# Optimization experiments

Measured on AMD Instinct MI355X. Metric: run time of the kernel, lower is better.

The kernel has to match this reference:

```python
import jax, jax.numpy as jnp
import numpy as np

B, L, DK, DV, H, DKL, DVL, R = 64, 4096, 128, 128, 4, 64, 128, 128


def setup_inputs() -> dict:
    key = jax.random.key(0)
    ks = jax.random.split(key, 7)
    K = jax.random.normal(ks[0], (B, L, DK), dtype=jnp.float32)
    V = jax.random.normal(ks[1], (B, L, DV), dtype=jnp.float32)
    mask = jax.random.uniform(ks[2], (B, L)) < 0.25
    mask = mask.at[:, 0].set(False)
    # Learned parameters (Wq is zeros at init in the original; use small random
    # values so the softmax is non-degenerate for correctness testing)
    Wq = jax.random.normal(ks[3], (H, DKL), dtype=jnp.float32) * 0.02
    Wk = jax.random.normal(ks[4], (DK, H, DKL), dtype=jnp.float32) / np.sqrt(DK)
    Wv = jax.random.normal(ks[5], (DV, H, DVL), dtype=jnp.float32) / np.sqrt(DV)
    Wo = jax.random.normal(ks[6], (H, DVL, R), dtype=jnp.float32) / np.sqrt(H * DVL)
    return {"K": K, "V": V, "mask": mask, "Wq": Wq, "Wk": Wk, "Wv": Wv, "Wo": Wo}


def reference(K, V, mask, Wq, Wk, Wv, Wo):
    # scale = 1/sqrt(dim_q), dim_q == dim_k
    scale = 1.0 / jnp.sqrt(jnp.asarray(K.shape[-1], K.dtype))
    Kp = jnp.einsum('bld,dhk->blhk', K, Wk)          # (B, L, H, DKL)
    Vp = jnp.einsum('ble,ehv->blhv', V, Wv)          # (B, L, H, DVL)
    QK = jnp.einsum('hk,blhk->blh', Wq, Kp)          # (B, L, H)
    QK = jnp.where(mask[..., None], -jnp.inf, QK)    # mask over set axis L
    w = jax.nn.softmax(scale * QK, axis=-2)          # softmax over L (dim=-2)
    # nanmean over the set axis (masked positions contribute w=0; NaN entries,
    # if present in V, are skipped exactly as torch.nanmean does)
    QKV = jnp.nanmean(w[..., None] * Vp, axis=-3)    # (B, H, DVL)
    return jnp.einsum('bhv,hvr->br', QKV, Wo)        # (B, R)
```

## Files before the change

### kernel.cpp

```cpp
#include <hip/hip_runtime.h>
#include <math.h>

#define BB   64
#define LL   4096
#define DKC  128
#define DVC  128
#define HC   4
#define DKLC 64
#define DVLC 128
#define RC   128

#define NCA  64
#define CA   64

typedef float f4v __attribute__((ext_vector_type(4)));
__device__ __forceinline__ float4 ntload4(const float4* p) {
    f4v v = __builtin_nontemporal_load((const f4v*)p);
    return make_float4(v.x, v.y, v.z, v.w);
}
__device__ __forceinline__ float dot4(float4 a, float4 b) {
    return a.x * b.x + a.y * b.y + a.z * b.z + a.w * b.w;
}

__global__ __launch_bounds__(512) void k_foldq(const float* __restrict__ Wq,
                                               const float* __restrict__ Wk,
                                               float* __restrict__ q) {
    int t = threadIdx.x;
    int h = t >> 7;
    int d = t & 127;
    float acc = 0.f;
#pragma unroll 8
    for (int k = 0; k < DKLC; ++k)
        acc += Wq[h * DKLC + k] * Wk[(d * HC + h) * DKLC + k];
    q[h * DKC + d] = acc;
}

__global__ __launch_bounds__(256) void k_fused(const float* __restrict__ K,
                                               const float* __restrict__ V,
                                               const int*   __restrict__ mask,
                                               const float* __restrict__ q,
                                               float* __restrict__ stats,
                                               float* __restrict__ partWV) {
    const int bid = blockIdx.x;
    const int b   = bid >> 6;
    const int a   = bid & (NCA - 1);
    const int l0  = a * CA;
    const int t   = threadIdx.x;
    const int w   = t >> 6;
    const int ln  = t & 63;
    const int lin = ln & 15;
    const int rh  = ln >> 5;
    const int rowbase = l0 + w * 16;

    const float4* Kb = (const float4*)(K + (long)b * LL * DKC);
    const float4* Vb = (const float4*)(V + (long)b * LL * DVC);

    float4 k0[4], k1[4];
#pragma unroll
    for (int p = 0; p < 4; ++p) {
        int rp = rowbase + p * 4 + (ln >> 4);
        k0[p] = ntload4(&Kb[rp * 32 + lin]);
        k1[p] = ntload4(&Kb[rp * 32 + 16 + lin]);
    }
    float4 vv[8];
#pragma unroll
    for (int it = 0; it < 8; ++it) {
        int rv = rowbase + it * 2 + rh;
        vv[it] = ntload4(&Vb[rv * 32 + (ln & 31)]);
    }
    int mk[4];
#pragma unroll
    for (int p = 0; p < 4; ++p)
        mk[p] = __builtin_nontemporal_load(mask + (long)b * LL + rowbase + p * 4 + (ln >> 4));

    float4 qa[HC], qb[HC];
#pragma unroll
    for (int h = 0; h < HC; ++h) {
        qa[h] = ((const float4*)q)[h * 32 + lin];
        qb[h] = ((const float4*)q)[h * 32 + 16 + lin];
    }

    const float scale = 0.08838834764831844f;
    float4 d[4];
#pragma unroll
    for (int p = 0; p < 4; ++p) {
        float4 dd;
        dd.x = dot4(k0[p], qa[0]) + dot4(k1[p], qb[0]);
        dd.y = dot4(k0[p], qa[1]) + dot4(k1[p], qb[1]);
        dd.z = dot4(k0[p], qa[2]) + dot4(k1[p], qb[2]);
        dd.w = dot4(k0[p], qa[3]) + dot4(k1[p], qb[3]);
#pragma unroll
        for (int off = 1; off <= 8; off <<= 1) {
            dd.x += __shfl_xor(dd.x, off);
            dd.y += __shfl_xor(dd.y, off);
            dd.z += __shfl_xor(dd.z, off);
            dd.w += __shfl_xor(dd.w, off);
        }
        d[p].x = mk[p] ? -INFINITY : dd.x * scale;
        d[p].y = mk[p] ? -INFINITY : dd.y * scale;
        d[p].z = mk[p] ? -INFINITY : dd.z * scale;
        d[p].w = mk[p] ? -INFINITY : dd.w * scale;
    }

    float4 m4;
    m4.x = fmaxf(fmaxf(d[0].x, d[1].x), fmaxf(d[2].x, d[3].x));
    m4.y = fmaxf(fmaxf(d[0].y, d[1].y), fmaxf(d[2].y, d[3].y));
    m4.z = fmaxf(fmaxf(d[0].z, d[1].z), fmaxf(d[2].z, d[3].z));
    m4.w = fmaxf(fmaxf(d[0].w, d[1].w), fmaxf(d[2].w, d[3].w));
#pragma unroll
    for (int off = 16; off <= 32; off <<= 1) {
        m4.x = fmaxf(m4.x, __shfl_xor(m4.x, off));
        m4.y = fmaxf(m4.y, __shfl_xor(m4.y, off));
        m4.z = fmaxf(m4.z, __shfl_xor(m4.z, off));
        m4.w = fmaxf(m4.w, __shfl_xor(m4.w, off));
    }
    float4 mu4;
    mu4.x = (m4.x == -INFINITY) ? 0.f : m4.x;
    mu4.y = (m4.y == -INFINITY) ? 0.f : m4.y;
    mu4.z = (m4.z == -INFINITY) ? 0.f : m4.z;
    mu4.w = (m4.w == -INFINITY) ? 0.f : m4.w;

    float4 pp[4];
#pragma unroll
    for (int p = 0; p < 4; ++p) {
        pp[p].x = expf(d[p].x - mu4.x);
        pp[p].y = expf(d[p].y - mu4.y);
        pp[p].z = expf(d[p].z - mu4.z);
        pp[p].w = expf(d[p].w - mu4.w);
    }
    float4 z4;
    z4.x = pp[0].x + pp[1].x + pp[2].x + pp[3].x;
    z4.y = pp[0].y + pp[1].y + pp[2].y + pp[3].y;
    z4.z = pp[0].z + pp[1].z + pp[2].z + pp[3].z;
    z4.w = pp[0].w + pp[1].w + pp[2].w + pp[3].w;
#pragma unroll
    for (int off = 16; off <= 32; off <<= 1) {
        z4.x += __shfl_xor(z4.x, off);
        z4.y += __shfl_xor(z4.y, off);
        z4.z += __shfl_xor(z4.z, off);
        z4.w += __shfl_xor(z4.w, off);
    }

    float4 acc[HC];
#pragma unroll
    for (int h = 0; h < HC; ++h) acc[h] = make_float4(0.f, 0.f, 0.f, 0.f);
#pragma unroll
    for (int it = 0; it < 8; ++it) {
        int src = (((2 * it) & 3) + rh) * 16 + lin;
        float4 w4;
        w4.x = __shfl(pp[it >> 1].x, src);
        w4.y = __shfl(pp[it >> 1].y, src);
        w4.z = __shfl(pp[it >> 1].z, src);
        w4.w = __shfl(pp[it >> 1].w, src);
        float4 v = vv[it];
        acc[0].x += w4.x*v.x; acc[0].y += w4.x*v.y; acc[0].z += w4.x*v.z; acc[0].w += w4.x*v.w;
        acc[1].x += w4.y*v.x; acc[1].y += w4.y*v.y; acc[1].z += w4.y*v.z; acc[1].w += w4.y*v.w;
        acc[2].x += w4.z*v.x; acc[2].y += w4.z*v.y; acc[2].z += w4.z*v.z; acc[2].w += w4.z*v.w;
        acc[3].x += w4.w*v.x; acc[3].y += w4.w*v.y; acc[3].z += w4.w*v.z; acc[3].w += w4.w*v.w;
    }

    __shared__ float4 wsm[4], wsz[4];
    __shared__ float4 red[4][32][HC];
    if (ln == 0) { wsm[w] = m4; wsz[w] = z4; }
    __syncthreads();

    float4 mb;
    mb.x = fmaxf(fmaxf(wsm[0].x, wsm[1].x), fmaxf(wsm[2].x, wsm[3].x));
    mb.y = fmaxf(fmaxf(wsm[0].y, wsm[1].y), fmaxf(wsm[2].y, wsm[3].y));
    mb.z = fmaxf(fmaxf(wsm[0].z, wsm[1].z), fmaxf(wsm[2].z, wsm[3].z));
    mb.w = fmaxf(fmaxf(wsm[0].w, wsm[1].w), fmaxf(wsm[2].w, wsm[3].w));
    float4 mub;
    mub.x = (mb.x == -INFINITY) ? 0.f : mb.x;
    mub.y = (mb.y == -INFINITY) ? 0.f : mb.y;
    mub.z = (mb.z == -INFINITY) ? 0.f : mb.z;
    mub.w = (mb.w == -INFINITY) ? 0.f : mb.w;
    float4 fw;
    fw.x = (wsm[w].x == -INFINITY) ? 0.f : expf(wsm[w].x - mub.x);
    fw.y = (wsm[w].y == -INFINITY) ? 0.f : expf(wsm[w].y - mub.y);
    fw.z = (wsm[w].z == -INFINITY) ? 0.f : expf(wsm[w].z - mub.z);
    fw.w = (wsm[w].w == -INFINITY) ? 0.f : expf(wsm[w].w - mub.w);
    acc[0].x *= fw.x; acc[0].y *= fw.x; acc[0].z *= fw.x; acc[0].w *= fw.x;
    acc[1].x *= fw.y; acc[1].y *= fw.y; acc[1].z *= fw.y; acc[1].w *= fw.y;
    acc[2].x *= fw.z; acc[2].y *= fw.z; acc[2].z *= fw.z; acc[2].w *= fw.z;
    acc[3].x *= fw.w; acc[3].y *= fw.w; acc[3].z *= fw.w; acc[3].w *= fw.w;

#pragma unroll
    for (int h = 0; h < HC; ++h) {
        acc[h].x += __shfl_xor(acc[h].x, 32);
        acc[h].y += __shfl_xor(acc[h].y, 32);
        acc[h].z += __shfl_xor(acc[h].z, 32);
        acc[h].w += __shfl_xor(acc[h].w, 32);
    }
    if (ln < 32) {
#pragma unroll
        for (int h = 0; h < HC; ++h) red[w][ln][h] = acc[h];
    }
    if (t == 0) {
        stats[(long)bid * 8 + 0] = mb.x;
        stats[(long)bid * 8 + 1] = mb.y;
        stats[(long)bid * 8 + 2] = mb.z;
        stats[(long)bid * 8 + 3] = mb.w;
        float zx = 0.f, zy = 0.f, zz = 0.f, zw = 0.f;
#pragma unroll
        for (int w2 = 0; w2 < 4; ++w2) {
            zx += ((wsm[w2].x == -INFINITY) ? 0.f : expf(wsm[w2].x - mub.x)) * wsz[w2].x;
            zy += ((wsm[w2].y == -INFINITY) ? 0.f : expf(wsm[w2].y - mub.y)) * wsz[w2].y;
            zz += ((wsm[w2].z == -INFINITY) ? 0.f : expf(wsm[w2].z - mub.z)) * wsz[w2].z;
            zw += ((wsm[w2].w == -INFINITY) ? 0.f : expf(wsm[w2].w - mub.w)) * wsz[w2].w;
        }
        stats[(long)bid * 8 + 4] = zx;
        stats[(long)bid * 8 + 5] = zy;
        stats[(long)bid * 8 + 6] = zz;
        stats[(long)bid * 8 + 7] = zw;
    }
    __syncthreads();
    if (t < 128) {
        int h = t >> 5, c = t & 31;
        float4 s0 = red[0][c][h], s1 = red[1][c][h];
        float4 s2 = red[2][c][h], s3 = red[3][c][h];
        float4 o;
        o.x = s0.x + s1.x + s2.x + s3.x;
        o.y = s0.y + s1.y + s2.y + s3.y;
        o.z = s0.z + s1.z + s2.z + s3.z;
        o.w = s0.w + s1.w + s2.w + s3.w;
        ((float4*)partWV)[((long)bid * HC + h) * (DVC / 4) + c] = o;
    }
}

__global__ __launch_bounds__(256) void k_out(const float* __restrict__ stats,
                                             const float* __restrict__ partWV,
                                             const float* __restrict__ Wv,
                                             const float* __restrict__ Wo,
                                             float* __restrict__ out) {
    int b = blockIdx.x;
    int t = threadIdx.x;
    __shared__ float WV[HC][DVC];
    __shared__ float QKV[HC * DVLC];
    __shared__ float sc[NCA][HC];
    __shared__ float zinv[HC];

    {
        int h2 = t >> 6, a = t & 63;
        float ma = stats[((long)b * NCA + a) * 8 + h2];
        float za = stats[((long)b * NCA + a) * 8 + 4 + h2];
        float m = ma;
#pragma unroll
        for (int off = 32; off; off >>= 1) m = fmaxf(m, __shfl_xor(m, off));
        float f  = (ma == -INFINITY) ? 0.f : expf(ma - m);
        sc[a][h2] = f;
        float fz = f * za;
#pragma unroll
        for (int off = 32; off; off >>= 1) fz += __shfl_xor(fz, off);
        if (a == 0) zinv[h2] = 1.0f / fz;
    }
    __syncthreads();

    for (int j = t; j < HC * DVC; j += 256) {
        int h = j >> 7, e = j & 127;
        float acc = 0.f;
#pragma unroll 8
        for (int p = 0; p < NCA; ++p)
            acc += sc[p][h] * partWV[(((long)b * NCA + p) * HC + h) * DVC + e];
        WV[h][e] = acc * zinv[h];
    }
    __syncthreads();

    for (int j = t; j < HC * DVLC; j += 256) {
        int h = j >> 7, vv = j & 127;
        float acc = 0.f;
#pragma unroll 8
        for (int e = 0; e < DVC; ++e)
            acc += WV[h][e] * Wv[(e * HC + h) * DVLC + vv];
        QKV[j] = acc * (1.0f / LL);
    }
    __syncthreads();

    for (int r = t; r < RC; r += 256) {
        float acc = 0.f;
#pragma unroll 8
        for (int i = 0; i < HC * DVLC; ++i)
            acc += QKV[i] * Wo[i * RC + r];
        out[b * RC + r] = acc;
    }
}

extern "C" void kernel_launch(void* const* d_in, const int* in_sizes, int n_in,
                              void* d_out, int out_size, void* d_ws, size_t ws_size,
                              hipStream_t stream) {
    (void)in_sizes; (void)n_in; (void)out_size; (void)ws_size;
    const float* K    = (const float*)d_in[0];
    const float* V    = (const float*)d_in[1];
    const int*   mask = (const int*)  d_in[2];
    const float* Wq   = (const float*)d_in[3];
    const float* Wk   = (const float*)d_in[4];
    const float* Wv   = (const float*)d_in[5];
    const float* Wo   = (const float*)d_in[6];
    float* out = (float*)d_out;

    float* q      = (float*)d_ws;
    float* stats  = q + 512;
    float* partWV = stats + (long)BB * NCA * 8;

    k_foldq<<<1, 512, 0, stream>>>(Wq, Wk, q);
    k_fused<<<BB * NCA, 256, 0, stream>>>(K, V, mask, q, stats, partWV);
    k_out<<<BB, 256, 0, stream>>>(stats, partWV, Wv, Wo, out);
}
```

Baseline: 77.76 us.

## Make each wave process a 64-row chunk with double-buffered loads and online softmax

Each wave now owns one full 64-row chunk of a batch, so the block count drops by four. It walks the chunk in four 16-row sub-chunks, keeping a running max and sum (online softmax) and double-buffering the K and V register loads so the next sub-chunk's loads are issued before the current one is computed. The block-level shared-memory reduction and __syncthreads are removed, and each wave writes its own stats and partial sums directly. The aim is to hide memory latency within a wave, at the cost of more registers (launch_bounds 256,2) and fewer blocks in flight.

```diff
diff --git a/kernel.cpp b/kernel.cpp
--- a/kernel.cpp
+++ b/kernel.cpp
@@ -11,7 +11,8 @@
 #define RC   128
 
 #define NCA  64
-#define CA   64
+#define NCH  4
+#define WPB  4
 
 typedef float f4v __attribute__((ext_vector_type(4)));
 __device__ __forceinline__ float4 ntload4(const float4* p) {
@@ -35,43 +36,27 @@
     q[h * DKC + d] = acc;
 }
 
-__global__ __launch_bounds__(256) void k_fused(const float* __restrict__ K,
-                                               const float* __restrict__ V,
-                                               const int*   __restrict__ mask,
-                                               const float* __restrict__ q,
-                                               float* __restrict__ stats,
-                                               float* __restrict__ partWV) {
-    const int bid = blockIdx.x;
-    const int b   = bid >> 6;
-    const int a   = bid & (NCA - 1);
-    const int l0  = a * CA;
+struct KBuf { float4 k0[4], k1[4]; int mk[4]; };
+struct VBuf { float4 vv[8]; };
+
+__global__ __launch_bounds__(256, 2) void k_fused(const float* __restrict__ K,
+                                                  const float* __restrict__ V,
+                                                  const int*   __restrict__ mask,
+                                                  const float* __restrict__ q,
+                                                  float* __restrict__ stats,
+                                                  float* __restrict__ partWV) {
     const int t   = threadIdx.x;
     const int w   = t >> 6;
     const int ln  = t & 63;
+    const int W   = blockIdx.x * WPB + w;
+    const int b   = W >> 6;
+    const int ws  = W & 63;
     const int lin = ln & 15;
     const int rh  = ln >> 5;
-    const int rowbase = l0 + w * 16;
-
-    const float4* Kb = (const float4*)(K + (long)b * LL * DKC);
-    const float4* Vb = (const float4*)(V + (long)b * LL * DVC);
-
-    float4 k0[4], k1[4];
-#pragma unroll
-    for (int p = 0; p < 4; ++p) {
-        int rp = rowbase + p * 4 + (ln >> 4);
-        k0[p] = ntload4(&Kb[rp * 32 + lin]);
-        k1[p] = ntload4(&Kb[rp * 32 + 16 + lin]);
-    }
-    float4 vv[8];
-#pragma unroll
-    for (int it = 0; it < 8; ++it) {
-        int rv = rowbase + it * 2 + rh;
-        vv[it] = ntload4(&Vb[rv * 32 + (ln & 31)]);
-    }
-    int mk[4];
-#pragma unroll
-    for (int p = 0; p < 4; ++p)
-        mk[p] = __builtin_nontemporal_load(mask + (long)b * LL + rowbase + p * 4 + (ln >> 4));
+
+    const float4* Kb    = (const float4*)(K + (long)b * LL * DKC);
+    const float4* Vb    = (const float4*)(V + (long)b * LL * DVC);
+    const int*    maskb = mask + (long)b * LL;
 
     float4 qa[HC], qb[HC];
 #pragma unroll
@@ -81,108 +66,131 @@
     }
 
     const float scale = 0.08838834764831844f;
-    float4 d[4];
-#pragma unroll
-    for (int p = 0; p < 4; ++p) {
-        float4 dd;
-        dd.x = dot4(k0[p], qa[0]) + dot4(k1[p], qb[0]);
-        dd.y = dot4(k0[p], qa[1]) + dot4(k1[p], qb[1]);
-        dd.z = dot4(k0[p], qa[2]) + dot4(k1[p], qb[2]);
-        dd.w = dot4(k0[p], qa[3]) + dot4(k1[p], qb[3]);
-#pragma unroll
-        for (int off = 1; off <= 8; off <<= 1) {
-            dd.x += __shfl_xor(dd.x, off);
-            dd.y += __shfl_xor(dd.y, off);
-            dd.z += __shfl_xor(dd.z, off);
-            dd.w += __shfl_xor(dd.w, off);
-        }
-        d[p].x = mk[p] ? -INFINITY : dd.x * scale;
-        d[p].y = mk[p] ? -INFINITY : dd.y * scale;
-        d[p].z = mk[p] ? -INFINITY : dd.z * scale;
-        d[p].w = mk[p] ? -INFINITY : dd.w * scale;
-    }
-
-    float4 m4;
-    m4.x = fmaxf(fmaxf(d[0].x, d[1].x), fmaxf(d[2].x, d[3].x));
-    m4.y = fmaxf(fmaxf(d[0].y, d[1].y), fmaxf(d[2].y, d[3].y));
-    m4.z = fmaxf(fmaxf(d[0].z, d[1].z), fmaxf(d[2].z, d[3].z));
-    m4.w = fmaxf(fmaxf(d[0].w, d[1].w), fmaxf(d[2].w, d[3].w));
-#pragma unroll
-    for (int off = 16; off <= 32; off <<= 1) {
-        m4.x = fmaxf(m4.x, __shfl_xor(m4.x, off));
-        m4.y = fmaxf(m4.y, __shfl_xor(m4.y, off));
-        m4.z = fmaxf(m4.z, __shfl_xor(m4.z, off));
-        m4.w = fmaxf(m4.w, __shfl_xor(m4.w, off));
-    }
-    float4 mu4;
-    mu4.x = (m4.x == -INFINITY) ? 0.f : m4.x;
-    mu4.y = (m4.y == -INFINITY) ? 0.f : m4.y;
-    mu4.z = (m4.z == -INFINITY) ? 0.f : m4.z;
-    mu4.w = (m4.w == -INFINITY) ? 0.f : m4.w;
-
+    float4 m_run = make_float4(-INFINITY, -INFINITY, -INFINITY, -INFINITY);
+    float4 Z_run = make_float4(0.f, 0.f, 0.f, 0.f);
+    float4 acc[HC];
+#pragma unroll
+    for (int h = 0; h < HC; ++h) acc[h] = make_float4(0.f, 0.f, 0.f, 0.f);
     float4 pp[4];
-#pragma unroll
-    for (int p = 0; p < 4; ++p) {
-        pp[p].x = expf(d[p].x - mu4.x);
-        pp[p].y = expf(d[p].y - mu4.y);
-        pp[p].z = expf(d[p].z - mu4.z);
-        pp[p].w = expf(d[p].w - mu4.w);
-    }
-    float4 z4;
-    z4.x = pp[0].x + pp[1].x + pp[2].x + pp[3].x;
-    z4.y = pp[0].y + pp[1].y + pp[2].y + pp[3].y;
-    z4.z = pp[0].z + pp[1].z + pp[2].z + pp[3].z;
-    z4.w = pp[0].w + pp[1].w + pp[2].w + pp[3].w;
-#pragma unroll
-    for (int off = 16; off <= 32; off <<= 1) {
-        z4.x += __shfl_xor(z4.x, off);
-        z4.y += __shfl_xor(z4.y, off);
-        z4.z += __shfl_xor(z4.z, off);
-        z4.w += __shfl_xor(z4.w, off);
-    }
-
-    float4 acc[HC];
-#pragma unroll
-    for (int h = 0; h < HC; ++h) acc[h] = make_float4(0.f, 0.f, 0.f, 0.f);
-#pragma unroll
-    for (int it = 0; it < 8; ++it) {
-        int src = (((2 * it) & 3) + rh) * 16 + lin;
-        float4 w4;
-        w4.x = __shfl(pp[it >> 1].x, src);
-        w4.y = __shfl(pp[it >> 1].y, src);
-        w4.z = __shfl(pp[it >> 1].z, src);
-        w4.w = __shfl(pp[it >> 1].w, src);
-        float4 v = vv[it];
-        acc[0].x += w4.x*v.x; acc[0].y += w4.x*v.y; acc[0].z += w4.x*v.z; acc[0].w += w4.x*v.w;
-        acc[1].x += w4.y*v.x; acc[1].y += w4.y*v.y; acc[1].z += w4.y*v.z; acc[1].w += w4.y*v.w;
-        acc[2].x += w4.z*v.x; acc[2].y += w4.z*v.y; acc[2].z += w4.z*v.z; acc[2].w += w4.z*v.w;
-        acc[3].x += w4.w*v.x; acc[3].y += w4.w*v.y; acc[3].z += w4.w*v.z; acc[3].w += w4.w*v.w;
-    }
-
-    __shared__ float4 wsm[4], wsz[4];
-    __shared__ float4 red[4][32][HC];
-    if (ln == 0) { wsm[w] = m4; wsz[w] = z4; }
-    __syncthreads();
-
-    float4 mb;
-    mb.x = fmaxf(fmaxf(wsm[0].x, wsm[1].x), fmaxf(wsm[2].x, wsm[3].x));
-    mb.y = fmaxf(fmaxf(wsm[0].y, wsm[1].y), fmaxf(wsm[2].y, wsm[3].y));
-    mb.z = fmaxf(fmaxf(wsm[0].z, wsm[1].z), fmaxf(wsm[2].z, wsm[3].z));
-    mb.w = fmaxf(fmaxf(wsm[0].w, wsm[1].w), fmaxf(wsm[2].w, wsm[3].w));
-    float4 mub;
-    mub.x = (mb.x == -INFINITY) ? 0.f : mb.x;
-    mub.y = (mb.y == -INFINITY) ? 0.f : mb.y;
-    mub.z = (mb.z == -INFINITY) ? 0.f : mb.z;
-    mub.w = (mb.w == -INFINITY) ? 0.f : mb.w;
-    float4 fw;
-    fw.x = (wsm[w].x == -INFINITY) ? 0.f : expf(wsm[w].x - mub.x);
-    fw.y = (wsm[w].y == -INFINITY) ? 0.f : expf(wsm[w].y - mub.y);
-    fw.z = (wsm[w].z == -INFINITY) ? 0.f : expf(wsm[w].z - mub.z);
-    fw.w = (wsm[w].w == -INFINITY) ? 0.f : expf(wsm[w].w - mub.w);
-    acc[0].x *= fw.x; acc[0].y *= fw.x; acc[0].z *= fw.x; acc[0].w *= fw.x;
-    acc[1].x *= fw.y; acc[1].y *= fw.y; acc[1].z *= fw.y; acc[1].w *= fw.y;
-    acc[2].x *= fw.z; acc[2].y *= fw.z; acc[2].z *= fw.z; acc[2].w *= fw.z;
-    acc[3].x *= fw.w; acc[3].y *= fw.w; acc[3].z *= fw.w; acc[3].w *= fw.w;
+
+    KBuf kA, kB;
+    VBuf vA, vB;
+
+    auto LK = [&](KBuf& Bf, int j) {
+        int rb = ws * 64 + j * 16;
+#pragma unroll
+        for (int p = 0; p < 4; ++p) {
+            int rp = rb + p * 4 + (ln >> 4);
+            Bf.k0[p] = ntload4(&Kb[rp * 32 + lin]);
+            Bf.k1[p] = ntload4(&Kb[rp * 32 + 16 + lin]);
+            Bf.mk[p] = __builtin_nontemporal_load(maskb + rp);
+        }
+    };
+    auto LV = [&](VBuf& Bf, int j) {
+        int rb = ws * 64 + j * 16;
+#pragma unroll
+        for (int it = 0; it < 8; ++it)
+            Bf.vv[it] = ntload4(&Vb[(rb + it * 2 + rh) * 32 + (ln & 31)]);
+    };
+    auto SCORE = [&](const KBuf& Bf) {
+        float4 d[4];
+#pragma unroll
+        for (int p = 0; p < 4; ++p) {
+            float4 dd;
+            dd.x = dot4(Bf.k0[p], qa[0]) + dot4(Bf.k1[p], qb[0]);
+            dd.y = dot4(Bf.k0[p], qa[1]) + dot4(Bf.k1[p], qb[1]);
+            dd.z = dot4(Bf.k0[p], qa[2]) + dot4(Bf.k1[p], qb[2]);
+            dd.w = dot4(Bf.k0[p], qa[3]) + dot4(Bf.k1[p], qb[3]);
+#pragma unroll
+            for (int off = 1; off <= 8; off <<= 1) {
+                dd.x += __shfl_xor(dd.x, off);
+                dd.y += __shfl_xor(dd.y, off);
+                dd.z += __shfl_xor(dd.z, off);
+                dd.w += __shfl_xor(dd.w, off);
+            }
+            d[p].x = Bf.mk[p] ? -INFINITY : dd.x * scale;
+            d[p].y = Bf.mk[p] ? -INFINITY : dd.y * scale;
+            d[p].z = Bf.mk[p] ? -INFINITY : dd.z * scale;
+            d[p].w = Bf.mk[p] ? -INFINITY : dd.w * scale;
+        }
+        float4 mc;
+        mc.x = fmaxf(fmaxf(d[0].x, d[1].x), fmaxf(d[2].x, d[3].x));
+        mc.y = fmaxf(fmaxf(d[0].y, d[1].y), fmaxf(d[2].y, d[3].y));
+        mc.z = fmaxf(fmaxf(d[0].z, d[1].z), fmaxf(d[2].z, d[3].z));
+        mc.w = fmaxf(fmaxf(d[0].w, d[1].w), fmaxf(d[2].w, d[3].w));
+#pragma unroll
+        for (int off = 16; off <= 32; off <<= 1) {
+            mc.x = fmaxf(mc.x, __shfl_xor(mc.x, off));
+            mc.y = fmaxf(mc.y, __shfl_xor(mc.y, off));
+            mc.z = fmaxf(mc.z, __shfl_xor(mc.z, off));
+            mc.w = fmaxf(mc.w, __shfl_xor(mc.w, off));
+        }
+        float4 mnew;
+        mnew.x = fmaxf(m_run.x, mc.x);
+        mnew.y = fmaxf(m_run.y, mc.y);
+        mnew.z = fmaxf(m_run.z, mc.z);
+        mnew.w = fmaxf(m_run.w, mc.w);
+        float4 mu;
+        mu.x = (mnew.x == -INFINITY) ? 0.f : mnew.x;
+        mu.y = (mnew.y == -INFINITY) ? 0.f : mnew.y;
+        mu.z = (mnew.z == -INFINITY) ? 0.f : mnew.z;
+        mu.w = (mnew.w == -INFINITY) ? 0.f : mnew.w;
+        float4 f;
+        f.x = expf(m_run.x - mu.x);
+        f.y = expf(m_run.y - mu.y);
+        f.z = expf(m_run.z - mu.z);
+        f.w = expf(m_run.w - mu.w);
+        acc[0].x *= f.x; acc[0].y *= f.x; acc[0].z *= f.x; acc[0].w *= f.x;
+        acc[1].x *= f.y; acc[1].y *= f.y; acc[1].z *= f.y; acc[1].w *= f.y;
+        acc[2].x *= f.z; acc[2].y *= f.z; acc[2].z *= f.z; acc[2].w *= f.z;
+        acc[3].x *= f.w; acc[3].y *= f.w; acc[3].z *= f.w; acc[3].w *= f.w;
+#pragma unroll
+        for (int p = 0; p < 4; ++p) {
+            pp[p].x = expf(d[p].x - mu.x);
+            pp[p].y = expf(d[p].y - mu.y);
+            pp[p].z = expf(d[p].z - mu.z);
+            pp[p].w = expf(d[p].w - mu.w);
+        }
+        float4 z;
+        z.x = pp[0].x + pp[1].x + pp[2].x + pp[3].x;
+        z.y = pp[0].y + pp[1].y + pp[2].y + pp[3].y;
+        z.z = pp[0].z + pp[1].z + pp[2].z + pp[3].z;
+        z.w = pp[0].w + pp[1].w + pp[2].w + pp[3].w;
+#pragma unroll
+        for (int off = 16; off <= 32; off <<= 1) {
+            z.x += __shfl_xor(z.x, off);
+            z.y += __shfl_xor(z.y, off);
+            z.z += __shfl_xor(z.z, off);
+            z.w += __shfl_xor(z.w, off);
+        }
+        Z_run.x = Z_run.x * f.x + z.x;
+        Z_run.y = Z_run.y * f.y + z.y;
+        Z_run.z = Z_run.z * f.z + z.z;
+        Z_run.w = Z_run.w * f.w + z.w;
+        m_run = mnew;
+    };
+    auto PV = [&](const VBuf& Bf) {
+#pragma unroll
+        for (int it = 0; it < 8; ++it) {
+            int src = (((2 * it) & 3) + rh) * 16 + lin;
+            float4 w4;
+            w4.x = __shfl(pp[it >> 1].x, src);
+            w4.y = __shfl(pp[it >> 1].y, src);
+            w4.z = __shfl(pp[it >> 1].z, src);
+            w4.w = __shfl(pp[it >> 1].w, src);
+            float4 v = Bf.vv[it];
+            acc[0].x += w4.x*v.x; acc[0].y += w4.x*v.y; acc[0].z += w4.x*v.z; acc[0].w += w4.x*v.w;
+            acc[1].x += w4.y*v.x; acc[1].y += w4.y*v.y; acc[1].z += w4.y*v.z; acc[1].w += w4.y*v.w;
+            acc[2].x += w4.z*v.x; acc[2].y += w4.z*v.y; acc[2].z += w4.z*v.z; acc[2].w += w4.z*v.w;
+            acc[3].x += w4.w*v.x; acc[3].y += w4.w*v.y; acc[3].z += w4.w*v.z; acc[3].w += w4.w*v.w;
+        }
+    };
+
+    LK(kA, 0); LV(vA, 0);
+    LK(kB, 1); SCORE(kA); LV(vB, 1); PV(vA);
+    LK(kA, 2); SCORE(kB); LV(vA, 2); PV(vB);
+    LK(kB, 3); SCORE(kA); LV(vB, 3); PV(vA);
+    SCORE(kB); PV(vB);
 
 #pragma unroll
     for (int h = 0; h < HC; ++h) {
@@ -191,39 +199,21 @@
         acc[h].z += __shfl_xor(acc[h].z, 32);
         acc[h].w += __shfl_xor(acc[h].w, 32);
     }
+    const long slot = (long)b * NCA + ws;
+    if (ln == 0) {
+        stats[slot * 8 + 0] = m_run.x;
+        stats[slot * 8 + 1] = m_run.y;
+        stats[slot * 8 + 2] = m_run.z;
+        stats[slot * 8 + 3] = m_run.w;
+        stats[slot * 8 + 4] = Z_run.x;
+        stats[slot * 8 + 5] = Z_run.y;
+        stats[slot * 8 + 6] = Z_run.z;
+        stats[slot * 8 + 7] = Z_run.w;
+    }
     if (ln < 32) {
 #pragma unroll
-        for (int h = 0; h < HC; ++h) red[w][ln][h] = acc[h];
-    }
-    if (t == 0) {
-        stats[(long)bid * 8 + 0] = mb.x;
-        stats[(long)bid * 8 + 1] = mb.y;
-        stats[(long)bid * 8 + 2] = mb.z;
-        stats[(long)bid * 8 + 3] = mb.w;
-        float zx = 0.f, zy = 0.f, zz = 0.f, zw = 0.f;
-#pragma unroll
-        for (int w2 = 0; w2 < 4; ++w2) {
-            zx += ((wsm[w2].x == -INFINITY) ? 0.f : expf(wsm[w2].x - mub.x)) * wsz[w2].x;
-            zy += ((wsm[w2].y == -INFINITY) ? 0.f : expf(wsm[w2].y - mub.y)) * wsz[w2].y;
-            zz += ((wsm[w2].z == -INFINITY) ? 0.f : expf(wsm[w2].z - mub.z)) * wsz[w2].z;
-            zw += ((wsm[w2].w == -INFINITY) ? 0.f : expf(wsm[w2].w - mub.w)) * wsz[w2].w;
-        }
-        stats[(long)bid * 8 + 4] = zx;
-        stats[(long)bid * 8 + 5] = zy;
-        stats[(long)bid * 8 + 6] = zz;
-        stats[(long)bid * 8 + 7] = zw;
-    }
-    __syncthreads();
-    if (t < 128) {
-        int h = t >> 5, c = t & 31;
-        float4 s0 = red[0][c][h], s1 = red[1][c][h];
-        float4 s2 = red[2][c][h], s3 = red[3][c][h];
-        float4 o;
-        o.x = s0.x + s1.x + s2.x + s3.x;
-        o.y = s0.y + s1.y + s2.y + s3.y;
-        o.z = s0.z + s1.z + s2.z + s3.z;
-        o.w = s0.w + s1.w + s2.w + s3.w;
-        ((float4*)partWV)[((long)bid * HC + h) * (DVC / 4) + c] = o;
+        for (int h = 0; h < HC; ++h)
+            ((float4*)partWV)[(slot * HC + h) * (DVC / 4) + ln] = acc[h];
     }
 }
 
@@ -302,6 +292,6 @@
     float* partWV = stats + (long)BB * NCA * 8;
 
     k_foldq<<<1, 512, 0, stream>>>(Wq, Wk, q);
-    k_fused<<<BB * NCA, 256, 0, stream>>>(K, V, mask, q, stats, partWV);
+    k_fused<<<BB * NCA / WPB, 256, 0, stream>>>(K, V, mask, q, stats, partWV);
     k_out<<<BB, 256, 0, stream>>>(stats, partWV, Wv, Wo, out);
 }
```

After: 84.26 us. 8.4% more time.
